# Performance work log

Measured on AMD Instinct MI355X. Metric: run time of the kernel, lower is better.

The kernel has to match this reference:

```python
import jax, jax.numpy as jnp
import numpy as np
import math

NUM_HEADS = 16


def build_hier_idx(seq_len):
    """Vectorized port of build_hierarchical_index_lookup_table.
    Returns [seq_len, log2(seq_len)] int32 neighbor indices into the
    concatenated [leaves | internal nodes] array of length 2*seq_len-1.
    For power-of-two seq_len every entry is valid (no -1s)."""
    assert seq_len & (seq_len - 1) == 0
    level_num = int(math.log2(seq_len))
    cur = np.arange(seq_len, dtype=np.int64)
    cols = []
    for lvl in range(level_num):
        if lvl == 0:
            nxt = cur ^ 1
        else:
            nxt = (cur // 2 + seq_len) ^ 1  # python precedence: (cur//2 + seq_len) ^ 1
        cols.append(nxt)
        cur = nxt
    return np.stack(cols, axis=1)  # [seq_len, level_num]


def setup_inputs() -> dict:
    key = jax.random.key(0)
    ks = jax.random.split(key, 9)
    B, N, D = 2, 2048, 1024
    s = 1.0 / math.sqrt(D)
    return {
        "query": jax.random.normal(ks[0], (B, N, D), jnp.float32),
        "key": jax.random.normal(ks[1], (B, N, D), jnp.float32),
        "value": jax.random.normal(ks[2], (B, N, D), jnp.float32),
        "y": jax.random.normal(ks[3], (B, N - 1, D), jnp.float32),
        "Wq": jax.random.normal(ks[4], (D, D), jnp.float32) * s,
        "Wk": jax.random.normal(ks[5], (D, D), jnp.float32) * s,
        "Wv": jax.random.normal(ks[6], (D, D), jnp.float32) * s,
        "Wo": jax.random.normal(ks[7], (D, D), jnp.float32) * s,
        "bo": jax.random.normal(ks[8], (D,), jnp.float32) * 0.01,
    }


def reference(query, key, value, y, Wq, Wk, Wv, Wo, bo):
    # Sparse path: L_Q == L_K == L_V and y is not None -> update_X_from_Y + out_proj_x.
    # key/value are unused in this branch (only their lengths are checked).
    B, N, D = query.shape
    H = NUM_HEADS
    Dh = D // H
    scale = 1.0 / math.sqrt(Dh)

    idx = jnp.asarray(build_hier_idx(N))          # [N, Lv], Lv = log2(N)

    xy = jnp.concatenate([query, y], axis=1)      # [B, 2N-1, D]
    Q = (query @ Wq.T).reshape(B, N, H, Dh).transpose(0, 2, 1, 3)   # [B,H,N,Dh]
    Kf = (xy @ Wk.T).reshape(B, -1, H, Dh).transpose(0, 2, 1, 3)    # [B,H,2N-1,Dh]
    Vf = (xy @ Wv.T).reshape(B, -1, H, Dh).transpose(0, 2, 1, 3)

    K_self = Kf[:, :, :N, :]                      # [B,H,N,Dh]
    V_self = Vf[:, :, :N, :]
    Kn = Kf[:, :, idx, :]                         # [B,H,N,Lv,Dh] gather over tree levels
    Vn = Vf[:, :, idx, :]

    self_logits = jnp.einsum('bhnd,bhnd->bhn', Q, K_self) * scale          # [B,H,N]
    nbr_logits = jnp.einsum('bhnd,bhnld->bhnl', Q, Kn) * scale             # [B,H,N,Lv]

    all_logits = jnp.concatenate([self_logits[..., None], nbr_logits], axis=-1)  # [B,H,N,1+Lv]
    all_v = jnp.concatenate([V_self[:, :, :, None, :], Vn], axis=3)              # [B,H,N,1+Lv,Dh]

    w = jax.nn.softmax(all_logits, axis=-1)
    out = jnp.einsum('bhnl,bhnld->bhnd', w, all_v)                               # [B,H,N,Dh]
    out = out.transpose(0, 2, 1, 3).reshape(B, N, D)
    return out @ Wo.T + bo
```

## Files before the change

### kernel.cpp

```cpp
#include <hip/hip_runtime.h>
#include <hip/hip_bf16.h>
#include <cstdint>
#include <cstddef>

#define B_ 2
#define N_ 2048
#define D_ 1024
#define H_ 16
#define DH_ 64
#define XYROWS 4095
#define NL 12
#define QKVN 3072

typedef __attribute__((ext_vector_type(8))) short bf16x8;
typedef __attribute__((ext_vector_type(4))) float f32x4;

__device__ __forceinline__ float asf(unsigned int u) {
    union { unsigned int i; float f; } v; v.i = u; return v.f;
}
__device__ __forceinline__ unsigned short f2bf(float f) {
    union { float f; unsigned int i; } v; v.f = f;
    unsigned int u = v.i;
    unsigned int r = u + 0x7FFFu + ((u >> 16) & 1u);
    return (unsigned short)(r >> 16);
}

__device__ __forceinline__ void ld8(const unsigned short* p, float* o) {
    uint4 u = *(const uint4*)p;
    o[0] = asf(u.x << 16); o[1] = asf(u.x & 0xffff0000u);
    o[2] = asf(u.y << 16); o[3] = asf(u.y & 0xffff0000u);
    o[4] = asf(u.z << 16); o[5] = asf(u.z & 0xffff0000u);
    o[6] = asf(u.w << 16); o[7] = asf(u.w & 0xffff0000u);
}

__device__ __forceinline__ void gload_lds16(const unsigned short* g, unsigned short* l) {
    __builtin_amdgcn_global_load_lds(
        (const __attribute__((address_space(1))) unsigned int*)g,
        (__attribute__((address_space(3))) unsigned int*)l,
        16, 0, 0);
}

__global__ void cvt_weights(const float* __restrict__ Wq, const float* __restrict__ Wk,
                            const float* __restrict__ Wv, const float* __restrict__ Wo,
                            unsigned short* __restrict__ wqkv, unsigned short* __restrict__ wob) {
    int c = blockIdx.x * blockDim.x + threadIdx.x;
    int which = c >> 17;
    int idx = c & 131071;
    const float* src = (which == 0) ? Wq : (which == 1) ? Wk : (which == 2) ? Wv : Wo;
    unsigned short* dst = (which < 3) ? (wqkv + (size_t)which * D_ * D_) : wob;
    size_t i = (size_t)idx * 8;
    float4 a = *(const float4*)(src + i);
    float4 b = *(const float4*)(src + i + 4);
    union { unsigned short us[8]; uint4 u4; } o;
    o.us[0] = f2bf(a.x); o.us[1] = f2bf(a.y); o.us[2] = f2bf(a.z); o.us[3] = f2bf(a.w);
    o.us[4] = f2bf(b.x); o.us[5] = f2bf(b.y); o.us[6] = f2bf(b.z); o.us[7] = f2bf(b.w);
    *(uint4*)(dst + i) = o.u4;
}

__global__ void build_xy(const float* __restrict__ q, const float* __restrict__ y,
                         unsigned short* __restrict__ xy) {
    int c = blockIdx.x * blockDim.x + threadIdx.x;
    int total = B_ * XYROWS * (D_ / 8);
    if (c >= total) return;
    int col8 = (c & (D_ / 8 - 1)) * 8;
    int rg = c >> 7;
    int b = (rg >= XYROWS) ? 1 : 0;
    int r = rg - b * XYROWS;
    const float* src;
    if (r < N_) src = q + ((size_t)b * N_ + r) * D_ + col8;
    else        src = y + ((size_t)b * (N_ - 1) + (r - N_)) * D_ + col8;
    float4 a = *(const float4*)(src);
    float4 bb = *(const float4*)(src + 4);
    union { unsigned short us[8]; uint4 u4; } o;
    o.us[0] = f2bf(a.x);  o.us[1] = f2bf(a.y);  o.us[2] = f2bf(a.z);  o.us[3] = f2bf(a.w);
    o.us[4] = f2bf(bb.x); o.us[5] = f2bf(bb.y); o.us[6] = f2bf(bb.z); o.us[7] = f2bf(bb.w);
    *(uint4*)(xy + (size_t)rg * D_ + col8) = o.u4;
}

template<bool OUTF32, bool BIAS>
__global__ __launch_bounds__(256, 2)
void gemm_bt(const unsigned short* __restrict__ A, const unsigned short* __restrict__ W,
             void* __restrict__ Cv, const float* __restrict__ bias, int M, int Nn) {
    constexpr int K = 1024, BK = 64;
    __shared__ __align__(16) unsigned short la[128 * 64];
    __shared__ __align__(16) unsigned short lb[128 * 64];

    int tid = threadIdx.x;
    int row0 = blockIdx.x * 128;
    int col0 = blockIdx.y * 128;
    int wave = tid >> 6, lane = tid & 63;
    int wm = wave >> 1, wn = wave & 1;
    int q4 = lane >> 4, r = lane & 15;

    int rseg = lane >> 3;
    int cseg = (lane & 7) * 8;

    f32x4 acc[4][4];
    f32x4 zero = {0.f, 0.f, 0.f, 0.f};
#pragma unroll
    for (int i = 0; i < 4; i++)
#pragma unroll
        for (int j = 0; j < 4; j++) acc[i][j] = zero;

    for (int k0 = 0; k0 < K; k0 += BK) {
#pragma unroll
        for (int p = 0; p < 4; p++) {
            int seg = wave * 4 + p;
            int rloc = seg * 8 + rseg;
            int ar = row0 + rloc; if (ar >= M) ar = M - 1;
            gload_lds16(A + (size_t)ar * K + k0 + cseg, &la[seg * 512]);
            gload_lds16(W + (size_t)(col0 + rloc) * K + k0 + cseg, &lb[seg * 512]);
        }
        __syncthreads();
#pragma unroll
        for (int ks = 0; ks < 2; ks++) {
            bf16x8 af[4], bfv[4];
#pragma unroll
            for (int i = 0; i < 4; i++)
                af[i] = *(const bf16x8*)(&la[(wm * 64 + i * 16 + r) * 64 + ks * 32 + q4 * 8]);
#pragma unroll
            for (int j = 0; j < 4; j++)
                bfv[j] = *(const bf16x8*)(&lb[(wn * 64 + j * 16 + r) * 64 + ks * 32 + q4 * 8]);
#pragma unroll
            for (int i = 0; i < 4; i++)
#pragma unroll
                for (int j = 0; j < 4; j++)
                    acc[i][j] = __builtin_amdgcn_mfma_f32_16x16x32_bf16(af[i], bfv[j], acc[i][j], 0, 0, 0);
        }
        __syncthreads();
    }

    float bv[4];
    if (BIAS) {
#pragma unroll
        for (int j = 0; j < 4; j++) bv[j] = bias[col0 + wn * 64 + j * 16 + r];
    }
#pragma unroll
    for (int i = 0; i < 4; i++) {
#pragma unroll
        for (int j = 0; j < 4; j++) {
            int col = col0 + wn * 64 + j * 16 + r;
#pragma unroll
            for (int reg = 0; reg < 4; reg++) {
                int row = row0 + wm * 64 + i * 16 + q4 * 4 + reg;
                if (row < M) {
                    float v = acc[i][j][reg];
                    if (BIAS) v += bv[j];
                    if (OUTF32)
                        ((float*)Cv)[(size_t)row * Nn + col] = v;
                    else
                        ((unsigned short*)Cv)[(size_t)row * Nn + col] = f2bf(v);
                }
            }
        }
    }
}

__global__ __launch_bounds__(256)
void attn_kernel(const unsigned short* __restrict__ QKV, unsigned short* __restrict__ O) {
    int t = threadIdx.x;
    int half = t >> 7;
    int c = t & 127;
    int b = blockIdx.y;
    int n = blockIdx.x * 2 + half;

    int rows[NL];
    rows[0] = n;
    int cur = n ^ 1;
    rows[1] = cur;
#pragma unroll
    for (int l = 1; l < 11; l++) {
        cur = ((cur >> 1) + N_) ^ 1;
        rows[l + 1] = cur;
    }

    const unsigned short* base = QKV + (size_t)b * XYROWS * QKVN;
    size_t c8 = (size_t)c * 8;

    float q[8];
    ld8(base + (size_t)n * QKVN + c8, q);

    float logits[NL];
#pragma unroll
    for (int j = 0; j < NL; j++) {
        float kv[8];
        ld8(base + (size_t)rows[j] * QKVN + D_ + c8, kv);
        float p = 0.f;
#pragma unroll
        for (int e = 0; e < 8; e++) p = fmaf(q[e], kv[e], p);
        p += __shfl_xor(p, 1);
        p += __shfl_xor(p, 2);
        p += __shfl_xor(p, 4);
        logits[j] = p * 0.125f;
    }

    float mx = logits[0];
#pragma unroll
    for (int j = 1; j < NL; j++) mx = fmaxf(mx, logits[j]);
    float s = 0.f, w[NL];
#pragma unroll
    for (int j = 0; j < NL; j++) { w[j] = __expf(logits[j] - mx); s += w[j]; }
    float inv = 1.f / s;

    float acc[8] = {0.f, 0.f, 0.f, 0.f, 0.f, 0.f, 0.f, 0.f};
#pragma unroll
    for (int j = 0; j < NL; j++) {
        float vv[8];
        ld8(base + (size_t)rows[j] * QKVN + 2 * D_ + c8, vv);
        float wj = w[j] * inv;
#pragma unroll
        for (int e = 0; e < 8; e++) acc[e] = fmaf(wj, vv[e], acc[e]);
    }

    union { unsigned short us[8]; uint4 u4; } o;
#pragma unroll
    for (int e = 0; e < 8; e++) o.us[e] = f2bf(acc[e]);
    *(uint4*)(O + ((size_t)b * N_ + n) * D_ + c8) = o.u4;
}

extern "C" void kernel_launch(void* const* d_in, const int* in_sizes, int n_in,
                              void* d_out, int out_size, void* d_ws, size_t ws_size,
                              hipStream_t stream) {
    const float* query = (const float*)d_in[0];
    const float* y  = (const float*)d_in[3];
    const float* Wq = (const float*)d_in[4];
    const float* Wk = (const float*)d_in[5];
    const float* Wv = (const float*)d_in[6];
    const float* Wo = (const float*)d_in[7];
    const float* bo = (const float*)d_in[8];
    float* out = (float*)d_out;

    char* ws = (char*)d_ws;
    size_t off = 0;
    auto alloc = [&](size_t bytes) {
        void* p = ws + off; off += (bytes + 255) & ~(size_t)255; return p;
    };
    unsigned short* xy   = (unsigned short*)alloc((size_t)B_ * XYROWS * D_ * 2 + 4096);
    unsigned short* wqkv = (unsigned short*)alloc((size_t)QKVN * D_ * 2);
    unsigned short* wob  = (unsigned short*)alloc((size_t)D_ * D_ * 2);
    unsigned short* QKV  = (unsigned short*)alloc((size_t)B_ * XYROWS * QKVN * 2);
    unsigned short* At   = (unsigned short*)alloc((size_t)B_ * N_ * D_ * 2);

    {
        int total = B_ * XYROWS * (D_ / 8);
        build_xy<<<(total + 255) / 256, 256, 0, stream>>>(query, y, xy);
        cvt_weights<<<2048, 256, 0, stream>>>(Wq, Wk, Wv, Wo, wqkv, wob);
    }
    {
        dim3 g((B_ * XYROWS + 127) / 128, QKVN / 128);
        gemm_bt<false, false><<<g, 256, 0, stream>>>(
            xy, wqkv, QKV, nullptr, B_ * XYROWS, QKVN);
    }
    {
        dim3 g(N_ / 2, B_);
        attn_kernel<<<g, 256, 0, stream>>>(QKV, At);
    }
    {
        dim3 g((B_ * N_) / 128, D_ / 128);
        gemm_bt<true, true><<<g, 256, 0, stream>>>(At, wob, out, bo, B_ * N_, D_);
    }
}
```

Measured before the change: 228.3 us.

## Fuse prep kernels, swizzle GEMM LDS, skip unused Q rows, shrink out-proj tile

Merges the xy-building and weight-conversion kernels into one launch. Adds an XOR swizzle to the GEMM's LDS layout so fragment reads avoid bank conflicts. The QKV GEMM now skips blocks that would compute Q columns for y rows, which are never used. The output projection uses 64-row tiles so the grid has more blocks. Together these cut wasted Q work and launch overhead and improve CU fill for the smaller GEMM.

```diff
diff --git a/kernel.cpp b/kernel.cpp
--- a/kernel.cpp
+++ b/kernel.cpp
@@ -40,89 +40,100 @@
         16, 0, 0);
 }
 
-__global__ void cvt_weights(const float* __restrict__ Wq, const float* __restrict__ Wk,
+__global__ void prep_kernel(const float* __restrict__ q, const float* __restrict__ y,
+                            const float* __restrict__ Wq, const float* __restrict__ Wk,
                             const float* __restrict__ Wv, const float* __restrict__ Wo,
+                            unsigned short* __restrict__ xy,
                             unsigned short* __restrict__ wqkv, unsigned short* __restrict__ wob) {
     int c = blockIdx.x * blockDim.x + threadIdx.x;
-    int which = c >> 17;
-    int idx = c & 131071;
-    const float* src = (which == 0) ? Wq : (which == 1) ? Wk : (which == 2) ? Wv : Wo;
-    unsigned short* dst = (which < 3) ? (wqkv + (size_t)which * D_ * D_) : wob;
-    size_t i = (size_t)idx * 8;
-    float4 a = *(const float4*)(src + i);
-    float4 b = *(const float4*)(src + i + 4);
-    union { unsigned short us[8]; uint4 u4; } o;
-    o.us[0] = f2bf(a.x); o.us[1] = f2bf(a.y); o.us[2] = f2bf(a.z); o.us[3] = f2bf(a.w);
-    o.us[4] = f2bf(b.x); o.us[5] = f2bf(b.y); o.us[6] = f2bf(b.z); o.us[7] = f2bf(b.w);
-    *(uint4*)(dst + i) = o.u4;
-}
-
-__global__ void build_xy(const float* __restrict__ q, const float* __restrict__ y,
-                         unsigned short* __restrict__ xy) {
-    int c = blockIdx.x * blockDim.x + threadIdx.x;
-    int total = B_ * XYROWS * (D_ / 8);
-    if (c >= total) return;
-    int col8 = (c & (D_ / 8 - 1)) * 8;
-    int rg = c >> 7;
-    int b = (rg >= XYROWS) ? 1 : 0;
-    int r = rg - b * XYROWS;
+    constexpr int TOTAL_XY = B_ * XYROWS * (D_ / 8);
+    constexpr int TOTAL_W  = 4 * 131072;
+    if (c >= TOTAL_XY + TOTAL_W) return;
     const float* src;
-    if (r < N_) src = q + ((size_t)b * N_ + r) * D_ + col8;
-    else        src = y + ((size_t)b * (N_ - 1) + (r - N_)) * D_ + col8;
+    unsigned short* dst;
+    if (c < TOTAL_XY) {
+        int col8 = (c & (D_ / 8 - 1)) * 8;
+        int rg = c >> 7;
+        int b = (rg >= XYROWS) ? 1 : 0;
+        int r = rg - b * XYROWS;
+        if (r < N_) src = q + ((size_t)b * N_ + r) * D_ + col8;
+        else        src = y + ((size_t)b * (N_ - 1) + (r - N_)) * D_ + col8;
+        dst = xy + (size_t)rg * D_ + col8;
+    } else {
+        int idx = c - TOTAL_XY;
+        int which = idx >> 17;
+        int sub = idx & 131071;
+        const float* w = (which == 0) ? Wq : (which == 1) ? Wk : (which == 2) ? Wv : Wo;
+        src = w + (size_t)sub * 8;
+        dst = ((which < 3) ? (wqkv + (size_t)which * D_ * D_) : wob) + (size_t)sub * 8;
+    }
     float4 a = *(const float4*)(src);
     float4 bb = *(const float4*)(src + 4);
     union { unsigned short us[8]; uint4 u4; } o;
     o.us[0] = f2bf(a.x);  o.us[1] = f2bf(a.y);  o.us[2] = f2bf(a.z);  o.us[3] = f2bf(a.w);
     o.us[4] = f2bf(bb.x); o.us[5] = f2bf(bb.y); o.us[6] = f2bf(bb.z); o.us[7] = f2bf(bb.w);
-    *(uint4*)(xy + (size_t)rg * D_ + col8) = o.u4;
-}
-
-template<bool OUTF32, bool BIAS>
+    *(uint4*)(dst) = o.u4;
+}
+
+template<int BM, bool OUTF32, bool BIAS, bool QSKIP>
 __global__ __launch_bounds__(256, 2)
 void gemm_bt(const unsigned short* __restrict__ A, const unsigned short* __restrict__ W,
              void* __restrict__ Cv, const float* __restrict__ bias, int M, int Nn) {
     constexpr int K = 1024, BK = 64;
-    __shared__ __align__(16) unsigned short la[128 * 64];
+    constexpr int IM = BM / 32;
+    __shared__ __align__(16) unsigned short la[BM * 64];
     __shared__ __align__(16) unsigned short lb[128 * 64];
 
+    int row0 = blockIdx.x * BM;
+    int col0 = blockIdx.y * 128;
+    if (QSKIP && col0 < 1024) {
+        int t = blockIdx.x;
+        if ((t >= 16 && t <= 30) || t >= 48) return;
+    }
     int tid = threadIdx.x;
-    int row0 = blockIdx.x * 128;
-    int col0 = blockIdx.y * 128;
     int wave = tid >> 6, lane = tid & 63;
     int wm = wave >> 1, wn = wave & 1;
     int q4 = lane >> 4, r = lane & 15;
 
-    int rseg = lane >> 3;
-    int cseg = (lane & 7) * 8;
-
-    f32x4 acc[4][4];
+    int rsub = lane >> 3;
+    int csw = ((lane & 7) ^ rsub) * 8;
+
+    f32x4 acc[IM][4];
     f32x4 zero = {0.f, 0.f, 0.f, 0.f};
 #pragma unroll
-    for (int i = 0; i < 4; i++)
+    for (int i = 0; i < IM; i++)
 #pragma unroll
         for (int j = 0; j < 4; j++) acc[i][j] = zero;
 
     for (int k0 = 0; k0 < K; k0 += BK) {
+#pragma unroll
+        for (int p = 0; p < IM; p++) {
+            int seg = wave * IM + p;
+            int ar = row0 + seg * 8 + rsub; if (ar >= M) ar = M - 1;
+            gload_lds16(A + (size_t)ar * K + k0 + csw, &la[seg * 512]);
+        }
 #pragma unroll
         for (int p = 0; p < 4; p++) {
             int seg = wave * 4 + p;
-            int rloc = seg * 8 + rseg;
-            int ar = row0 + rloc; if (ar >= M) ar = M - 1;
-            gload_lds16(A + (size_t)ar * K + k0 + cseg, &la[seg * 512]);
-            gload_lds16(W + (size_t)(col0 + rloc) * K + k0 + cseg, &lb[seg * 512]);
+            gload_lds16(W + (size_t)(col0 + seg * 8 + rsub) * K + k0 + csw, &lb[seg * 512]);
         }
         __syncthreads();
 #pragma unroll
         for (int ks = 0; ks < 2; ks++) {
-            bf16x8 af[4], bfv[4];
-#pragma unroll
-            for (int i = 0; i < 4; i++)
-                af[i] = *(const bf16x8*)(&la[(wm * 64 + i * 16 + r) * 64 + ks * 32 + q4 * 8]);
-#pragma unroll
-            for (int j = 0; j < 4; j++)
-                bfv[j] = *(const bf16x8*)(&lb[(wn * 64 + j * 16 + r) * 64 + ks * 32 + q4 * 8]);
-#pragma unroll
-            for (int i = 0; i < 4; i++)
+            int cidx = ks * 4 + q4;
+            bf16x8 af[IM], bfv[4];
+#pragma unroll
+            for (int i = 0; i < IM; i++) {
+                int rr = wm * (BM / 2) + i * 16 + r;
+                af[i] = *(const bf16x8*)(&la[rr * 64 + ((cidx ^ (rr & 7)) << 3)]);
+            }
+#pragma unroll
+            for (int j = 0; j < 4; j++) {
+                int rb = wn * 64 + j * 16 + r;
+                bfv[j] = *(const bf16x8*)(&lb[rb * 64 + ((cidx ^ (rb & 7)) << 3)]);
+            }
+#pragma unroll
+            for (int i = 0; i < IM; i++)
 #pragma unroll
                 for (int j = 0; j < 4; j++)
                     acc[i][j] = __builtin_amdgcn_mfma_f32_16x16x32_bf16(af[i], bfv[j], acc[i][j], 0, 0, 0);
@@ -136,13 +147,13 @@
         for (int j = 0; j < 4; j++) bv[j] = bias[col0 + wn * 64 + j * 16 + r];
     }
 #pragma unroll
-    for (int i = 0; i < 4; i++) {
+    for (int i = 0; i < IM; i++) {
 #pragma unroll
         for (int j = 0; j < 4; j++) {
             int col = col0 + wn * 64 + j * 16 + r;
 #pragma unroll
             for (int reg = 0; reg < 4; reg++) {
-                int row = row0 + wm * 64 + i * 16 + q4 * 4 + reg;
+                int row = row0 + wm * (BM / 2) + i * 16 + q4 * 4 + reg;
                 if (row < M) {
                     float v = acc[i][j][reg];
                     if (BIAS) v += bv[j];
@@ -241,14 +252,11 @@
     unsigned short* QKV  = (unsigned short*)alloc((size_t)B_ * XYROWS * QKVN * 2);
     unsigned short* At   = (unsigned short*)alloc((size_t)B_ * N_ * D_ * 2);
 
-    {
-        int total = B_ * XYROWS * (D_ / 8);
-        build_xy<<<(total + 255) / 256, 256, 0, stream>>>(query, y, xy);
-        cvt_weights<<<2048, 256, 0, stream>>>(Wq, Wk, Wv, Wo, wqkv, wob);
-    }
+    prep_kernel<<<6144, 256, 0, stream>>>(query, y, Wq, Wk, Wv, Wo, xy, wqkv, wob);
+
     {
         dim3 g((B_ * XYROWS + 127) / 128, QKVN / 128);
-        gemm_bt<false, false><<<g, 256, 0, stream>>>(
+        gemm_bt<128, false, false, true><<<g, 256, 0, stream>>>(
             xy, wqkv, QKV, nullptr, B_ * XYROWS, QKVN);
     }
     {
@@ -256,7 +264,7 @@
         attn_kernel<<<g, 256, 0, stream>>>(QKV, At);
     }
     {
-        dim3 g((B_ * N_) / 128, D_ / 128);
-        gemm_bt<true, true><<<g, 256, 0, stream>>>(At, wob, out, bo, B_ * N_, D_);
-    }
-}
+        dim3 g((B_ * N_) / 64, D_ / 128);
+        gemm_bt<64, true, true, false><<<g, 256, 0, stream>>>(At, wob, out, bo, B_ * N_, D_);
+    }
+}
```

New measurement: 201.0 us. 12.0% less time.
